# Kernel tuning notes

Hardware: AMD Instinct MI355X
Metric: run time of the kernel (lower is better)

Reference implementation:

```python
import jax, jax.numpy as jnp
import numpy as np

NEG = -1e6  # matches torch masked value of -1000000.0
EPS = 1e-5


def setup_inputs() -> dict:
    key = jax.random.key(0)
    k1, k2, k3, k4, k5, k6 = jax.random.split(key, 6)
    B, H, L, D = 2, 16, 2048, 128
    BH = B * H
    return {
        "queries": jax.random.normal(k1, (BH, L, D), dtype=jnp.float32),
        "keys": jax.random.normal(k2, (BH, L, D), dtype=jnp.float32),
        "values": jax.random.normal(k3, (BH, L, D), dtype=jnp.float32),
        "q_mult": jax.random.normal(k4, (B, L, D), dtype=jnp.float32),
        "kv_mult": jax.random.normal(k5, (B, L, D), dtype=jnp.float32),
        "valid_lens": jax.random.randint(k6, (BH,), 0, L, dtype=jnp.int64),
        "num_heads": 16,
    }


def reference(queries, keys, values, q_mult, kv_mult, valid_lens, num_heads):
    # queries/keys/values: [BH, L, d]; q_mult/kv_mult: [B, L, d_m]; valid_lens: [BH]
    d = queries.shape[-1]
    Lk = keys.shape[1]
    scale = 1.0 / jnp.sqrt(jnp.asarray(d, dtype=queries.dtype))
    scores = jnp.einsum('bqd,bkd->bqk', queries, keys) * scale  # [BH, Lq, Lk]

    # custom additive multiplicative-interaction term, Frobenius-normalized per batch element
    mult_ = jnp.einsum('bqd,bkd->bqk', q_mult, kv_mult)  # [B, Lq, Lk]
    fro = jnp.sqrt(jnp.sum(mult_ * mult_, axis=(1, 2), keepdims=True))
    mult_ = mult_ / (fro + EPS)
    mult_ = jnp.repeat(mult_, num_heads, axis=0)  # [BH, Lq, Lk]

    # masked softmax over keys: valid_lens is per-(batch*head), broadcast over queries
    key_mask = jnp.arange(Lk)[None, None, :] < valid_lens[:, None, None]  # [BH, 1, Lk]
    scores = jnp.where(key_mask, scores, NEG)
    attn = jax.nn.softmax(scores, axis=-1) + mult_  # after_softmax=True path

    # dropout is identity (p=0 / eval)
    return jnp.einsum('bqk,bkd->bqd', attn, values)
```

## Files before the change

### kernel.cpp

```cpp
#include <hip/hip_runtime.h>


typedef __attribute__((ext_vector_type(8))) __bf16 bf16x8;
typedef __attribute__((ext_vector_type(16))) float f32x16;
typedef __attribute__((ext_vector_type(4))) unsigned int u32x4;

#define DEV static __device__ __forceinline__

constexpr int LL = 2048, DD = 128, BH = 32;
constexpr float SCALE = 0.08838834764831845f;
constexpr float SCALE2 = 0.12752736105f;
constexpr float NEGV = -1e6f;

DEV unsigned pkb(float a, float b) {
  union { __bf16 h[2]; unsigned u; } x;
  x.h[0] = (__bf16)a; x.h[1] = (__bf16)b;
  return x.u;
}
DEV f32x16 mfma32(bf16x8 a, bf16x8 b, f32x16 c) {
  return __builtin_amdgcn_mfma_f32_32x32x16_bf16(a, b, c, 0, 0, 0);
}
DEV void gl16(const void* g, void* l) {
  __builtin_amdgcn_global_load_lds(
      (const __attribute__((address_space(1))) unsigned int*)g,
      (__attribute__((address_space(3))) unsigned int*)l, 16, 0, 0);
}

__global__ __launch_bounds__(256)
void mega_pre(const float* __restrict__ K, const float* __restrict__ V,
              const float* __restrict__ qm, const float* __restrict__ km,
              char* __restrict__ Kb, char* __restrict__ Vt,
              float* __restrict__ Gq, float* __restrict__ Gk,
              float* __restrict__ Mp) {
  __shared__ __align__(16) char smem[16384];
  const int bx = blockIdx.x, tid = threadIdx.x;

  if (bx < 512) {
    float (*skv)[64] = (float(*)[64])smem;
    float (*sv)[128] = (float(*)[128])(smem + 4096);
    int bh = bx & 31, b = bh >> 4, kc = (bx >> 5) & 7, z = (bx >> 8) & 1;
    int l0 = kc * 256;
    int j0 = (tid & 31) * 4, i0 = (tid >> 5) * 8;
    float acc[8][4];
#pragma unroll
    for (int i = 0; i < 8; ++i)
#pragma unroll
      for (int qq = 0; qq < 4; ++qq) acc[i][qq] = 0.f;
    for (int c = 0; c < 16; ++c) {
      __syncthreads();
      {
        int rr = tid >> 4, c4 = (tid & 15) * 4;
        *(float4*)&skv[rr][c4] =
            *(const float4*)(km + (size_t)(b * LL + l0 + c * 16 + rr) * DD + z * 64 + c4);
#pragma unroll
        for (int x = 0; x < 2; ++x) {
          int id2 = x * 256 + tid;
          int r2 = id2 >> 5, c42 = (id2 & 31) * 4;
          *(float4*)&sv[r2][c42] =
              *(const float4*)(V + (size_t)(bh * LL + l0 + c * 16 + r2) * DD + c42);
        }
      }
      __syncthreads();
#pragma unroll
      for (int ll = 0; ll < 16; ++ll) {
        float4 a = *(const float4*)&sv[ll][j0];
        float4 k0 = *(const float4*)&skv[ll][i0];
        float4 k1 = *(const float4*)&skv[ll][i0 + 4];
        float kk[8] = {k0.x, k0.y, k0.z, k0.w, k1.x, k1.y, k1.z, k1.w};
#pragma unroll
        for (int ii = 0; ii < 8; ++ii) {
          acc[ii][0] += kk[ii] * a.x;
          acc[ii][1] += kk[ii] * a.y;
          acc[ii][2] += kk[ii] * a.z;
          acc[ii][3] += kk[ii] * a.w;
        }
      }
    }
    float* dst = Mp + (((size_t)bh * 8 + kc) << 14) + (size_t)(z * 64 + i0) * 128 + j0;
#pragma unroll
    for (int ii = 0; ii < 8; ++ii)
      *(float4*)(dst + (size_t)ii * 128) = *(float4*)&acc[ii][0];

  } else if (bx < 640) {
    float (*s)[128] = (float(*)[128])smem;
    int g = bx - 512;
    int ib = g & 7, lc = (g >> 3) & 3, wb = g >> 5;
    int which = wb >> 1, b = wb & 1;
    const float* A = (which ? km : qm) + (size_t)b * LL * DD;
    float* G = (which ? Gk : Gq) + (size_t)b * DD * DD;
    int i0 = ib * 16 + (tid >> 7) * 8, j = tid & 127;
    int l0 = lc * 512;
    float acc[8];
#pragma unroll
    for (int i = 0; i < 8; ++i) acc[i] = 0.f;
    for (int ch = 0; ch < 16; ++ch) {
      __syncthreads();
#pragma unroll
      for (int i = 0; i < 4; ++i) {
        int c = i * 256 + tid;
        int row = c >> 5, c4 = (c & 31) * 4;
        *(float4*)&s[row][c4] =
            *(const float4*)(A + (size_t)(l0 + ch * 32 + row) * DD + c4);
      }
      __syncthreads();
#pragma unroll
      for (int ll = 0; ll < 32; ++ll) {
        float aj = s[ll][j];
#pragma unroll
        for (int ii = 0; ii < 8; ++ii) acc[ii] += s[ll][i0 + ii] * aj;
      }
    }
#pragma unroll
    for (int ii = 0; ii < 8; ++ii)
      atomicAdd(&G[(size_t)(i0 + ii) * DD + j], acc[ii]);

  } else if (bx < 1664) {
    int pk = bx - 640;
#pragma unroll
    for (int i = 0; i < 4; ++i) {
      int cid = i * 262144 + pk * 256 + tid;
      int h = cid >> 15, k = (cid >> 4) & 2047, c = cid & 15;
      const float* p = K + ((size_t)h * LL + k) * DD + c * 8;
      float4 x0 = *(const float4*)p, x1 = *(const float4*)(p + 4);
      u32x4 v;
      v.x = pkb(x0.x, x0.y); v.y = pkb(x0.z, x0.w);
      v.z = pkb(x1.x, x1.y); v.w = pkb(x1.z, x1.w);
      char* dst = Kb + (((size_t)h * 64 + (k >> 5)) << 13) + ((k & 31) << 8) +
                  ((c ^ (k & 15)) << 4);
      *(u32x4*)dst = v;
    }

  } else {
    float (*sV)[128] = (float(*)[128])smem;
    int pv = bx - 1664;
    int h = pv >> 6, kt = pv & 63;
    const float* src = V + ((size_t)h * LL + kt * 32) * DD;
#pragma unroll
    for (int i = 0; i < 4; ++i) {
      int c = i * 256 + tid;
      int row = c >> 5, c4 = (c & 31) * 4;
      *(float4*)&sV[row][c4] = *(const float4*)(src + (size_t)row * DD + c4);
    }
    __syncthreads();
    char* dstb = Vt + (((size_t)h * 64 + kt) << 13);
#pragma unroll
    for (int i = 0; i < 2; ++i) {
      int cid = i * 256 + tid;
      int f = cid >> 6, l = cid & 63;
      int d = (f >> 1) * 32 + (l & 31);
      int k0 = ((f & 1) * 2 + (l >> 5)) * 8;
      u32x4 v;
      v.x = pkb(sV[k0 + 0][d], sV[k0 + 1][d]);
      v.y = pkb(sV[k0 + 2][d], sV[k0 + 3][d]);
      v.z = pkb(sV[k0 + 4][d], sV[k0 + 5][d]);
      v.w = pkb(sV[k0 + 6][d], sV[k0 + 7][d]);
      *(u32x4*)(dstb + f * 1024 + l * 16) = v;
    }
  }
}

__global__ __launch_bounds__(256)
void k_post(const float* __restrict__ Gq, const float* __restrict__ Gk,
            float* __restrict__ fro, const float* __restrict__ Mp,
            char* __restrict__ MT) {
  int bx = blockIdx.x, tid = threadIdx.x;
  if (bx < 2) {
    int b = bx;
    const float* gq = Gq + (size_t)b * DD * DD;
    const float* gk = Gk + (size_t)b * DD * DD;
    float acc = 0.f;
    for (int i = tid; i < DD * DD; i += 256) acc += gq[i] * gk[i];
#pragma unroll
    for (int m = 32; m; m >>= 1) acc += __shfl_xor(acc, m);
    __shared__ float sbuf[4];
    if ((tid & 63) == 0) sbuf[tid >> 6] = acc;
    __syncthreads();
    if (tid == 0) fro[b] = sqrtf(sbuf[0] + sbuf[1] + sbuf[2] + sbuf[3]);
  } else {
    int g = bx - 2;
    int bh = g >> 2, kq = (g & 3) * 32;
    int k = kq + (tid >> 3), d0 = (tid & 7) * 16;
    float acc[16];
#pragma unroll
    for (int i = 0; i < 16; ++i) acc[i] = 0.f;
#pragma unroll
    for (int s = 0; s < 8; ++s) {
      const float* p = Mp + (((size_t)bh * 8 + s) << 14) + (size_t)k * 128 + d0;
#pragma unroll
      for (int i = 0; i < 4; ++i) {
        float4 v = *(const float4*)(p + i * 4);
        acc[4 * i + 0] += v.x; acc[4 * i + 1] += v.y;
        acc[4 * i + 2] += v.z; acc[4 * i + 3] += v.w;
      }
    }
    char* dst = MT + (size_t)bh * 32768;
#pragma unroll
    for (int j = 0; j < 16; ++j) {
      int d = d0 + j;
      union { __bf16 h; unsigned short u; } cv;
      cv.h = (__bf16)acc[j];
      *(unsigned short*)(dst + d * 256 + (((k >> 3) ^ (d & 15)) << 4) + (k & 7) * 2) = cv.u;
    }
  }
}

__global__ __launch_bounds__(128, 2)
void k_flash2(const char* __restrict__ KbG, const char* __restrict__ VtG,
              const char* __restrict__ MT, const float* __restrict__ fro,
              const float* __restrict__ Qf, const float* __restrict__ qmf,
              const int* __restrict__ vl, float* __restrict__ out) {
  __shared__ __align__(16) char lds[32768];

  const int qt = blockIdx.x, bh = blockIdx.y, b = bh >> 4;
  const int tid = threadIdx.x, w = tid >> 6, lane = tid & 63;
  const int r32 = lane & 31, hi = lane >> 5;
  const int vlen = vl[bh];
  const size_t base = (size_t)bh * LL * DD;
  const int q = qt * 32 + r32;
  char* ldsW = lds + w * 16384;

  bf16x8 qfr[8];
#pragma unroll
  for (int ks = 0; ks < 8; ++ks) {
    const float* p = Qf + base + (size_t)q * DD + ks * 16 + hi * 8;
    float4 x0 = *(const float4*)p, x1 = *(const float4*)(p + 4);
    union { unsigned u[4]; bf16x8 v; } u;
    u.u[0] = pkb(x0.x * SCALE2, x0.y * SCALE2);
    u.u[1] = pkb(x0.z * SCALE2, x0.w * SCALE2);
    u.u[2] = pkb(x1.x * SCALE2, x1.y * SCALE2);
    u.u[3] = pkb(x1.z * SCALE2, x1.w * SCALE2);
    qfr[ks] = u.v;
  }

  f32x16 o[4];
#pragma unroll
  for (int dt = 0; dt < 4; ++dt)
#pragma unroll
    for (int e = 0; e < 16; ++e) o[dt][e] = 0.f;
  float lrun = 0.f;

  int nt = (vlen == 0) ? 64 : ((vlen + 31) >> 5);
  const float mskv = (vlen == 0) ? 0.f : NEGV;

  const char* kb = KbG + (((size_t)bh * 64) << 13);
  const char* vb = VtG + (((size_t)bh * 64) << 13);

  auto stageK = [&](int t, int c2) {
    const char* gk = kb + ((size_t)t << 13) + lane * 16;
    char* lk = ldsW + c2 * 8192 + lane * 16;
#pragma unroll
    for (int i = 0; i < 8; ++i) gl16(gk + i * 1024, lk + i * 1024);
  };
  auto loadV = [&](int t, u32x4* vr) {
    const char* gv = vb + ((size_t)t << 13) + lane * 16;
#pragma unroll
    for (int f = 0; f < 8; ++f)
      vr[f] = *(const u32x4*)(gv + f * 1024);
  };

  auto compute = [&](const char* Kl, const u32x4* vr, int kbase) {
    f32x16 s0;
#pragma unroll
    for (int e = 0; e < 16; ++e) s0[e] = 0.f;
    __builtin_amdgcn_s_setprio(1);
#pragma unroll
    for (int ks = 0; ks < 8; ++ks) {
      bf16x8 a0 = *(const bf16x8*)(Kl + r32 * 256 + (((2 * ks + hi) ^ (r32 & 15)) << 4));
      s0 = mfma32(a0, qfr[ks], s0);
    }
    __builtin_amdgcn_s_setprio(0);

    if (kbase + 32 > vlen) {
#pragma unroll
      for (int e = 0; e < 16; ++e) {
        int k0 = kbase + (e & 3) + 8 * (e >> 2) + 4 * hi;
        if (k0 >= vlen) s0[e] = mskv;
      }
    }
#pragma unroll
    for (int e = 0; e < 16; ++e) s0[e] = exp2f(s0[e]);
    f32x16 sm = s0;
#pragma unroll
    for (int st = 8; st; st >>= 1)
#pragma unroll
      for (int e = 0; e < st; ++e) sm[e] += sm[e + st];
    lrun += sm[0];

    bf16x8 PA[2];
#pragma unroll
    for (int ks = 0; ks < 2; ++ks) {
      int bb = ks * 8;
      unsigned x1 = pkb(s0[bb + 0], s0[bb + 1]);
      unsigned x2 = pkb(s0[bb + 2], s0[bb + 3]);
      unsigned y1 = pkb(s0[bb + 4], s0[bb + 5]);
      unsigned y2 = pkb(s0[bb + 6], s0[bb + 7]);
      unsigned sx1 = __shfl_xor(x1, 32), sx2 = __shfl_xor(x2, 32);
      unsigned sy1 = __shfl_xor(y1, 32), sy2 = __shfl_xor(y2, 32);
      union { unsigned u[4]; bf16x8 v; } pu;
      pu.u[0] = hi ? sy1 : x1;
      pu.u[1] = hi ? sy2 : x2;
      pu.u[2] = hi ? y1 : sx1;
      pu.u[3] = hi ? y2 : sx2;
      PA[ks] = pu.v;
    }
    __builtin_amdgcn_s_setprio(1);
#pragma unroll
    for (int dt = 0; dt < 4; ++dt)
#pragma unroll
      for (int ks = 0; ks < 2; ++ks) {
        union { u32x4 w; bf16x8 v; } cv;
        cv.w = vr[dt * 2 + ks];
        o[dt] = mfma32(cv.v, PA[ks], o[dt]);
      }
    __builtin_amdgcn_s_setprio(0);
  };

  {
    u32x4 vA[8], vB[8];
    int t = w;
    if (t < nt) {
      stageK(t, 0);
      loadV(t, vA);
      while (true) {
        if (t + 2 < nt) {
          stageK(t + 2, 1); loadV(t + 2, vB);
          asm volatile("s_waitcnt vmcnt(16)" ::: "memory");
        } else {
          asm volatile("s_waitcnt vmcnt(0)" ::: "memory");
        }
        __builtin_amdgcn_sched_barrier(0);
        compute(ldsW, vA, t * 32);
        t += 2; if (t >= nt) break;

        if (t + 2 < nt) {
          stageK(t + 2, 0); loadV(t + 2, vA);
          asm volatile("s_waitcnt vmcnt(16)" ::: "memory");
        } else {
          asm volatile("s_waitcnt vmcnt(0)" ::: "memory");
        }
        __builtin_amdgcn_sched_barrier(0);
        compute(ldsW + 8192, vB, t * 32);
        t += 2; if (t >= nt) break;
      }
    }
  }

  float ltw = lrun + __shfl_xor(lrun, 32);
  float* oshare = (float*)(lds + 16384);
  float* lshare = (float*)lds;
  if (w == 1) {
#pragma unroll
    for (int dt = 0; dt < 4; ++dt)
#pragma unroll
      for (int e = 0; e < 16; ++e)
        oshare[(dt * 16 + e) * 64 + lane] = o[dt][e];
  }
  __syncthreads();
  if (w == 1) {
    if (hi == 0) lshare[r32] = ltw;
  }
  __syncthreads();
  if (w == 1) return;

  float lt = ltw + lshare[r32];
  float inv = 1.f / lt;
#pragma unroll
  for (int dt = 0; dt < 4; ++dt)
#pragma unroll
    for (int e = 0; e < 16; ++e)
      o[dt][e] = (o[dt][e] + oshare[(dt * 16 + e) * 64 + lane]) * inv;

  {
    float invf = 1.f / (fro[b] + 1e-5f);
    bf16x8 qb[8];
#pragma unroll
    for (int ks = 0; ks < 8; ++ks) {
      const float* p = qmf + ((size_t)b * LL + q) * DD + ks * 16 + hi * 8;
      float4 x0 = *(const float4*)p, x1 = *(const float4*)(p + 4);
      union { unsigned u[4]; bf16x8 v; } u;
      u.u[0] = pkb(x0.x * invf, x0.y * invf);
      u.u[1] = pkb(x0.z * invf, x0.w * invf);
      u.u[2] = pkb(x1.x * invf, x1.y * invf);
      u.u[3] = pkb(x1.z * invf, x1.w * invf);
      qb[ks] = u.v;
    }
    const char* MTb = MT + (size_t)bh * 32768;
#pragma unroll
    for (int kc = 0; kc < 8; ++kc)
#pragma unroll
      for (int dt = 0; dt < 4; ++dt) {
        bf16x8 av = *(const bf16x8*)(MTb + (dt * 32 + r32) * 256 +
                                     (((2 * kc + hi) ^ (r32 & 15)) << 4));
        o[dt] = mfma32(av, qb[kc], o[dt]);
      }
  }

  float* op = out + base + (size_t)q * DD;
#pragma unroll
  for (int dt = 0; dt < 4; ++dt)
#pragma unroll
    for (int rq = 0; rq < 4; ++rq) {
      float4 v;
      v.x = o[dt][4 * rq + 0];
      v.y = o[dt][4 * rq + 1];
      v.z = o[dt][4 * rq + 2];
      v.w = o[dt][4 * rq + 3];
      *(float4*)(op + dt * 32 + rq * 8 + hi * 4) = v;
    }
}

__global__ __launch_bounds__(128, 2)
void k_flashF(const float* __restrict__ Qf, const float* __restrict__ Kf,
              const float* __restrict__ Vf, const int* __restrict__ vl,
              float* __restrict__ out) {
  __shared__ __align__(16) char lds[16384];
  const int qt = blockIdx.x, bh = blockIdx.y;
  const int tid = threadIdx.x, w = tid >> 6, lane = tid & 63;
  const int r32 = lane & 31, hi = lane >> 5;
  const int vlen = vl[bh];
  const size_t base = (size_t)bh * LL * DD;
  const int q = qt * 64 + w * 32 + r32;

  bf16x8 qfr[8];
#pragma unroll
  for (int ks = 0; ks < 8; ++ks) {
    const float* p = Qf + base + (size_t)q * DD + ks * 16 + hi * 8;
    float4 x0 = *(const float4*)p, x1 = *(const float4*)(p + 4);
    union { unsigned u[4]; bf16x8 v; } u;
    u.u[0] = pkb(x0.x * SCALE, x0.y * SCALE);
    u.u[1] = pkb(x0.z * SCALE, x0.w * SCALE);
    u.u[2] = pkb(x1.x * SCALE, x1.y * SCALE);
    u.u[3] = pkb(x1.z * SCALE, x1.w * SCALE);
    qfr[ks] = u.v;
  }

  f32x16 o[4];
#pragma unroll
  for (int dt = 0; dt < 4; ++dt)
#pragma unroll
    for (int e = 0; e < 16; ++e) o[dt][e] = 0.f;
  float mrun = -3e38f, lrun = 0.f;
  int nt = (vlen == 0) ? 64 : ((vlen + 31) >> 5);

  char* Kl = lds;
  char* Vl = lds + 8192;
  for (int t = 0; t < nt; ++t) {
    int kbase = t * 32;
    __syncthreads();
#pragma unroll
    for (int i = 0; i < 4; ++i) {
      int c = i * 128 + tid;
      int kk = c >> 4, sl = c & 15;
      const float* p = Kf + base + (size_t)(kbase + kk) * DD + sl * 8;
      float4 x0 = *(const float4*)p, x1 = *(const float4*)(p + 4);
      u32x4 v;
      v.x = pkb(x0.x, x0.y); v.y = pkb(x0.z, x0.w);
      v.z = pkb(x1.x, x1.y); v.w = pkb(x1.z, x1.w);
      *(u32x4*)(Kl + (kk << 8) + ((sl ^ (kk & 15)) << 4)) = v;
    }
#pragma unroll
    for (int i = 0; i < 4; ++i) {
      int c = i * 128 + tid;
      int d = c >> 2, kk8 = c & 3;
      float t0[8];
#pragma unroll
      for (int j = 0; j < 8; ++j)
        t0[j] = Vf[base + (size_t)(kbase + kk8 * 8 + j) * DD + d];
      u32x4 v;
      v.x = pkb(t0[0], t0[1]); v.y = pkb(t0[2], t0[3]);
      v.z = pkb(t0[4], t0[5]); v.w = pkb(t0[6], t0[7]);
      *(u32x4*)(Vl + d * 64 + ((kk8 ^ ((d >> 1) & 3)) << 4)) = v;
    }
    __syncthreads();

    f32x16 s0;
#pragma unroll
    for (int e = 0; e < 16; ++e) s0[e] = 0.f;
#pragma unroll
    for (int ks = 0; ks < 8; ++ks) {
      bf16x8 a0 = *(const bf16x8*)(Kl + r32 * 256 + (((2 * ks + hi) ^ (r32 & 15)) << 4));
      s0 = mfma32(a0, qfr[ks], s0);
    }
    if (kbase + 32 > vlen) {
#pragma unroll
      for (int e = 0; e < 16; ++e) {
        int k0 = kbase + (e & 3) + 8 * (e >> 2) + 4 * hi;
        if (k0 >= vlen) s0[e] = NEGV;
      }
    }
    f32x16 mx = s0;
#pragma unroll
    for (int st = 8; st; st >>= 1)
#pragma unroll
      for (int e = 0; e < st; ++e) mx[e] = fmaxf(mx[e], mx[e + st]);
    float pm = fmaxf(mx[0], __shfl_xor(mx[0], 32));
    if (!__all(pm <= mrun + 8.f)) {
      float mn = fmaxf(mrun, pm);
      float al = __expf(mrun - mn);
      lrun *= al;
#pragma unroll
      for (int dt = 0; dt < 4; ++dt)
#pragma unroll
        for (int e = 0; e < 16; ++e) o[dt][e] *= al;
      mrun = mn;
    }
#pragma unroll
    for (int e = 0; e < 16; ++e) s0[e] = __expf(s0[e] - mrun);
    f32x16 sm = s0;
#pragma unroll
    for (int st = 8; st; st >>= 1)
#pragma unroll
      for (int e = 0; e < st; ++e) sm[e] += sm[e + st];
    lrun += sm[0];

    bf16x8 PA[2];
#pragma unroll
    for (int ks = 0; ks < 2; ++ks) {
      int bb = ks * 8;
      unsigned x1 = pkb(s0[bb + 0], s0[bb + 1]);
      unsigned x2 = pkb(s0[bb + 2], s0[bb + 3]);
      unsigned y1 = pkb(s0[bb + 4], s0[bb + 5]);
      unsigned y2 = pkb(s0[bb + 6], s0[bb + 7]);
      unsigned sx1 = __shfl_xor(x1, 32), sx2 = __shfl_xor(x2, 32);
      unsigned sy1 = __shfl_xor(y1, 32), sy2 = __shfl_xor(y2, 32);
      union { unsigned u[4]; bf16x8 v; } pu;
      pu.u[0] = hi ? sy1 : x1;
      pu.u[1] = hi ? sy2 : x2;
      pu.u[2] = hi ? y1 : sx1;
      pu.u[3] = hi ? y2 : sx2;
      PA[ks] = pu.v;
    }
#pragma unroll
    for (int dt = 0; dt < 4; ++dt)
#pragma unroll
      for (int ks = 0; ks < 2; ++ks) {
        bf16x8 av = *(const bf16x8*)(Vl + (dt * 32 + r32) * 64 +
                                     (((2 * ks + hi) ^ ((r32 >> 1) & 3)) << 4));
        o[dt] = mfma32(av, PA[ks], o[dt]);
      }
    __syncthreads();
  }

  float lt = lrun + __shfl_xor(lrun, 32);
  float inv = 1.f / lt;
  float* op = out + base + (size_t)q * DD;
#pragma unroll
  for (int dt = 0; dt < 4; ++dt)
#pragma unroll
    for (int rq = 0; rq < 4; ++rq) {
      float4 v;
      v.x = o[dt][4 * rq + 0] * inv;
      v.y = o[dt][4 * rq + 1] * inv;
      v.z = o[dt][4 * rq + 2] * inv;
      v.w = o[dt][4 * rq + 3] * inv;
      *(float4*)(op + dt * 32 + rq * 8 + hi * 4) = v;
    }
}

__global__ void k_gram(const float* __restrict__ qm, const float* __restrict__ km,
                       float* __restrict__ Gq, float* __restrict__ Gk) {
  int which = blockIdx.z >> 1, b = blockIdx.z & 1;
  const float* A = (which ? km : qm) + (size_t)b * LL * DD;
  float* G = (which ? Gk : Gq) + (size_t)b * DD * DD;
  int i0 = blockIdx.x * 8;
  int l0 = blockIdx.y * 512;
  __shared__ float s[32][128];
  float acc[8];
#pragma unroll
  for (int i = 0; i < 8; ++i) acc[i] = 0.f;
  for (int ch = 0; ch < 16; ++ch) {
    __syncthreads();
    for (int rr = 0; rr < 32; ++rr)
      s[rr][threadIdx.x] = A[(size_t)(l0 + ch * 32 + rr) * DD + threadIdx.x];
    __syncthreads();
    for (int ll = 0; ll < 32; ++ll) {
      float aj = s[ll][threadIdx.x];
#pragma unroll
      for (int ii = 0; ii < 8; ++ii) acc[ii] += s[ll][i0 + ii] * aj;
    }
  }
#pragma unroll
  for (int ii = 0; ii < 8; ++ii)
    atomicAdd(&G[(size_t)(i0 + ii) * DD + threadIdx.x], acc[ii]);
}

__global__ void k_fro(const float* __restrict__ Gq, const float* __restrict__ Gk,
                      float* __restrict__ fro) {
  int b = blockIdx.x;
  const float* gq = Gq + (size_t)b * DD * DD;
  const float* gk = Gk + (size_t)b * DD * DD;
  float acc = 0.f;
  for (int i = threadIdx.x; i < DD * DD; i += 256) acc += gq[i] * gk[i];
#pragma unroll
  for (int m = 32; m; m >>= 1) acc += __shfl_xor(acc, m);
  __shared__ float sbuf[4];
  if ((threadIdx.x & 63) == 0) sbuf[threadIdx.x >> 6] = acc;
  __syncthreads();
  if (threadIdx.x == 0) fro[b] = sqrtf(sbuf[0] + sbuf[1] + sbuf[2] + sbuf[3]);
}

__global__ void k_M_atomic(const float* __restrict__ km, const float* __restrict__ Vf,
                           float* __restrict__ M) {
  int bh = blockIdx.x, b = bh >> 4;
  int l0 = blockIdx.y * 128;
  __shared__ float skv[16][128];
  __shared__ float sv[16][128];
  int j0 = (threadIdx.x & 31) * 4;
  int i0 = (threadIdx.x >> 5) * 16;
  float acc[16][4];
#pragma unroll
  for (int i = 0; i < 16; ++i)
#pragma unroll
    for (int qq = 0; qq < 4; ++qq) acc[i][qq] = 0.f;
  for (int c = 0; c < 8; ++c) {
    __syncthreads();
    for (int x = 0; x < 8; ++x) {
      int idx = x * 256 + threadIdx.x;
      int rr = idx >> 7, cc = idx & 127;
      skv[rr][cc] = km[(size_t)(b * LL + l0 + c * 16 + rr) * DD + cc];
      sv[rr][cc] = Vf[(size_t)(bh * LL + l0 + c * 16 + rr) * DD + cc];
    }
    __syncthreads();
    for (int ll = 0; ll < 16; ++ll) {
      float a0 = sv[ll][j0], a1 = sv[ll][j0 + 1];
      float a2 = sv[ll][j0 + 2], a3 = sv[ll][j0 + 3];
#pragma unroll
      for (int ii = 0; ii < 16; ++ii) {
        float kv = skv[ll][i0 + ii];
        acc[ii][0] += kv * a0;
        acc[ii][1] += kv * a1;
        acc[ii][2] += kv * a2;
        acc[ii][3] += kv * a3;
      }
    }
  }
#pragma unroll
  for (int ii = 0; ii < 16; ++ii)
#pragma unroll
    for (int qq = 0; qq < 4; ++qq)
      atomicAdd(&M[(size_t)bh * DD * DD + (size_t)(i0 + ii) * DD + j0 + qq],
                acc[ii][qq]);
}

__global__ void k_multadd(const float* __restrict__ qm, const float* __restrict__ M,
                          const float* __restrict__ fro, float* __restrict__ out) {
  int bh = blockIdx.y, b = bh >> 4;
  int l = blockIdx.x * 128 + (threadIdx.x & 127);
  int dh = (threadIdx.x >> 7) * 64;
  float inv = 1.0f / (fro[b] + 1e-5f);
  const float* qrow = qm + ((size_t)b * LL + l) * DD;
  const float* Mb = M + (size_t)bh * DD * DD + dh;
  float acc[64];
#pragma unroll
  for (int i = 0; i < 64; ++i) acc[i] = 0.f;
  for (int k = 0; k < 128; ++k) {
    float qv = qrow[k];
    const float4* m4 = (const float4*)(Mb + (size_t)k * DD);
#pragma unroll
    for (int i = 0; i < 16; ++i) {
      float4 mm = m4[i];
      acc[4 * i + 0] += qv * mm.x;
      acc[4 * i + 1] += qv * mm.y;
      acc[4 * i + 2] += qv * mm.z;
      acc[4 * i + 3] += qv * mm.w;
    }
  }
  float* op = out + ((size_t)bh * LL + l) * DD + dh;
#pragma unroll
  for (int i = 0; i < 16; ++i) {
    float4 ov = ((float4*)op)[i];
    ov.x += acc[4 * i + 0] * inv;
    ov.y += acc[4 * i + 1] * inv;
    ov.z += acc[4 * i + 2] * inv;
    ov.w += acc[4 * i + 3] * inv;
    ((float4*)op)[i] = ov;
  }
}

extern "C" void kernel_launch(void* const* d_in, const int* in_sizes, int n_in,
                              void* d_out, int out_size, void* d_ws, size_t ws_size,
                              hipStream_t stream) {
  (void)in_sizes; (void)n_in; (void)out_size;
  const float* Q = (const float*)d_in[0];
  const float* K = (const float*)d_in[1];
  const float* V = (const float*)d_in[2];
  const float* qm = (const float*)d_in[3];
  const float* km = (const float*)d_in[4];
  const int* vl = (const int*)d_in[5];
  float* out = (float*)d_out;

  char* ws = (char*)d_ws;
  const size_t off_Gq = 0;
  const size_t off_Gk = 131072;
  const size_t off_fro = 262144;
  const size_t off_MT = 294912;
  const size_t off_Kb = off_MT + 1048576;
  const size_t szb = (size_t)BH * LL * DD * 2;
  const size_t off_Vt = off_Kb + szb;
  const size_t off_end = off_Vt + szb;
  bool fits = ws_size >= off_end;

  float* Gq = (float*)(ws + off_Gq);
  float* Gk = (float*)(ws + off_Gk);
  float* fro = (float*)(ws + off_fro);
  char* MT = ws + off_MT;

  if (fits) {
    float* Mp = (float*)d_out;
    hipMemsetAsync(ws, 0, off_fro + 256, stream);
    mega_pre<<<3712, 256, 0, stream>>>(K, V, qm, km, ws + off_Kb, ws + off_Vt,
                                       Gq, Gk, Mp);
    k_post<<<130, 256, 0, stream>>>(Gq, Gk, fro, Mp, MT);
    k_flash2<<<dim3(64, 32), 128, 0, stream>>>(ws + off_Kb, ws + off_Vt, MT, fro,
                                               Q, qm, vl, out);
  } else {
    float* Mw = (float*)(ws + off_MT);
    hipMemsetAsync(ws, 0, off_MT + 2097152, stream);
    k_gram<<<dim3(16, 4, 4), 128, 0, stream>>>(qm, km, Gq, Gk);
    k_fro<<<2, 256, 0, stream>>>(Gq, Gk, fro);
    k_flashF<<<dim3(32, 32), 128, 0, stream>>>(Q, K, V, vl, out);
    k_M_atomic<<<dim3(32, 16), 256, 0, stream>>>(km, V, Mw);
    k_multadd<<<dim3(16, 32), 256, 0, stream>>>(qm, Mw, fro, out);
  }
}
```

Before: 158.2 us.

## Single-buffer K in LDS and pack partial O to bf16 for higher occupancy

Each wave now keeps one K tile in LDS instead of two, so the kernel's LDS drops from 32 KB to 16 KB and launch bounds rise from 2 to 4 blocks per CU. The prefetch of the next K/V tile is moved to just after the QK^T MFMAs have finished reading LDS (an lgkmcnt wait). It then overlaps only with the softmax and PV work, and each phase starts with a full vmcnt(0) wait. To fit the cross-wave reduction into the smaller LDS, wave 1's partial output is stored as bf16 pairs rather than fp32. The aim is better latency hiding from more resident waves, at the cost of a shorter prefetch distance, extra rounding of the partial accumulator, and possible register pressure under the tighter bound.

```diff
diff --git a/kernel.cpp b/kernel.cpp
--- a/kernel.cpp
+++ b/kernel.cpp
@@ -204,12 +204,12 @@
   }
 }
 
-__global__ __launch_bounds__(128, 2)
+__global__ __launch_bounds__(128, 4)
 void k_flash2(const char* __restrict__ KbG, const char* __restrict__ VtG,
               const char* __restrict__ MT, const float* __restrict__ fro,
               const float* __restrict__ Qf, const float* __restrict__ qmf,
               const int* __restrict__ vl, float* __restrict__ out) {
-  __shared__ __align__(16) char lds[32768];
+  __shared__ __align__(16) char lds[16384];
 
   const int qt = blockIdx.x, bh = blockIdx.y, b = bh >> 4;
   const int tid = threadIdx.x, w = tid >> 6, lane = tid & 63;
@@ -217,7 +217,7 @@
   const int vlen = vl[bh];
   const size_t base = (size_t)bh * LL * DD;
   const int q = qt * 32 + r32;
-  char* ldsW = lds + w * 16384;
+  char* ldsW = lds + w * 8192;
 
   bf16x8 qfr[8];
 #pragma unroll
@@ -245,9 +245,9 @@
   const char* kb = KbG + (((size_t)bh * 64) << 13);
   const char* vb = VtG + (((size_t)bh * 64) << 13);
 
-  auto stageK = [&](int t, int c2) {
+  auto stageK = [&](int t) {
     const char* gk = kb + ((size_t)t << 13) + lane * 16;
-    char* lk = ldsW + c2 * 8192 + lane * 16;
+    char* lk = ldsW + lane * 16;
 #pragma unroll
     for (int i = 0; i < 8; ++i) gl16(gk + i * 1024, lk + i * 1024);
   };
@@ -258,18 +258,27 @@
       vr[f] = *(const u32x4*)(gv + f * 1024);
   };
 
-  auto compute = [&](const char* Kl, const u32x4* vr, int kbase) {
+  auto phase = [&](const u32x4* vcur, u32x4* vnext, int t) {
+    asm volatile("s_waitcnt vmcnt(0)" ::: "memory");
+    __builtin_amdgcn_sched_barrier(0);
     f32x16 s0;
 #pragma unroll
     for (int e = 0; e < 16; ++e) s0[e] = 0.f;
     __builtin_amdgcn_s_setprio(1);
 #pragma unroll
     for (int ks = 0; ks < 8; ++ks) {
-      bf16x8 a0 = *(const bf16x8*)(Kl + r32 * 256 + (((2 * ks + hi) ^ (r32 & 15)) << 4));
+      bf16x8 a0 = *(const bf16x8*)(ldsW + r32 * 256 + (((2 * ks + hi) ^ (r32 & 15)) << 4));
       s0 = mfma32(a0, qfr[ks], s0);
     }
     __builtin_amdgcn_s_setprio(0);
-
+    asm volatile("s_waitcnt lgkmcnt(0)" ::: "memory");
+    __builtin_amdgcn_sched_barrier(0);
+    if (t + 2 < nt) {
+      stageK(t + 2);
+      loadV(t + 2, vnext);
+    }
+
+    int kbase = t * 32;
     if (kbase + 32 > vlen) {
 #pragma unroll
       for (int e = 0; e < 16; ++e) {
@@ -309,7 +318,7 @@
 #pragma unroll
       for (int ks = 0; ks < 2; ++ks) {
         union { u32x4 w; bf16x8 v; } cv;
-        cv.w = vr[dt * 2 + ks];
+        cv.w = vcur[dt * 2 + ks];
         o[dt] = mfma32(cv.v, PA[ks], o[dt]);
       }
     __builtin_amdgcn_s_setprio(0);
@@ -319,41 +328,26 @@
     u32x4 vA[8], vB[8];
     int t = w;
     if (t < nt) {
-      stageK(t, 0);
+      stageK(t);
       loadV(t, vA);
       while (true) {
-        if (t + 2 < nt) {
-          stageK(t + 2, 1); loadV(t + 2, vB);
-          asm volatile("s_waitcnt vmcnt(16)" ::: "memory");
-        } else {
-          asm volatile("s_waitcnt vmcnt(0)" ::: "memory");
-        }
-        __builtin_amdgcn_sched_barrier(0);
-        compute(ldsW, vA, t * 32);
+        phase(vA, vB, t);
         t += 2; if (t >= nt) break;
-
-        if (t + 2 < nt) {
-          stageK(t + 2, 0); loadV(t + 2, vA);
-          asm volatile("s_waitcnt vmcnt(16)" ::: "memory");
-        } else {
-          asm volatile("s_waitcnt vmcnt(0)" ::: "memory");
-        }
-        __builtin_amdgcn_sched_barrier(0);
-        compute(ldsW + 8192, vB, t * 32);
+        phase(vB, vA, t);
         t += 2; if (t >= nt) break;
       }
     }
   }
 
   float ltw = lrun + __shfl_xor(lrun, 32);
-  float* oshare = (float*)(lds + 16384);
+  unsigned* osh = (unsigned*)(lds + 8192);
   float* lshare = (float*)lds;
   if (w == 1) {
 #pragma unroll
     for (int dt = 0; dt < 4; ++dt)
 #pragma unroll
-      for (int e = 0; e < 16; ++e)
-        oshare[(dt * 16 + e) * 64 + lane] = o[dt][e];
+      for (int e2 = 0; e2 < 8; ++e2)
+        osh[(dt * 8 + e2) * 64 + lane] = pkb(o[dt][2 * e2], o[dt][2 * e2 + 1]);
   }
   __syncthreads();
   if (w == 1) {
@@ -367,8 +361,12 @@
 #pragma unroll
   for (int dt = 0; dt < 4; ++dt)
 #pragma unroll
-    for (int e = 0; e < 16; ++e)
-      o[dt][e] = (o[dt][e] + oshare[(dt * 16 + e) * 64 + lane]) * inv;
+    for (int e2 = 0; e2 < 8; ++e2) {
+      union { unsigned u; __bf16 h[2]; } cv;
+      cv.u = osh[(dt * 8 + e2) * 64 + lane];
+      o[dt][2 * e2]     = (o[dt][2 * e2]     + (float)cv.h[0]) * inv;
+      o[dt][2 * e2 + 1] = (o[dt][2 * e2 + 1] + (float)cv.h[1]) * inv;
+    }
 
   {
     float invf = 1.f / (fro[b] + 1e-5f);
```

Result: slower. 380.9 us (+140.7%).
